# Optimization experiments

Hardware: AMD Instinct MI355X
Metric: run time of the kernel (lower is better)

Reference implementation:

```python
import jax, jax.numpy as jnp
import numpy as np

C = 343.0      # speed of sound (init kwarg c)
F = 16         # number of frequency channels (len(omega))
H = 128        # MLP hidden width
N = 131072     # collocation points


def _mlp(coords, W1, b1, W2, b2, W3, b3):
    # coords: [..., 3] -> [..., 2F] (first F = real part, last F = imag part)
    h = jnp.tanh(coords @ W1 + b1)
    h = jnp.tanh(h @ W2 + b2)
    return h @ W3 + b3


def setup_inputs() -> dict:
    key = jax.random.key(0)
    ks = jax.random.split(key, 4)
    inputs = jax.random.normal(ks[0], (N, 3), dtype=jnp.float32)
    # omega = 2*pi*f for f = 100..1600 Hz (matches init kwarg list)
    omega = 2.0 * jnp.pi * 100.0 * jnp.arange(1, F + 1, dtype=jnp.float32)
    s_in = 1.0 / np.sqrt(3.0)
    s_h = 1.0 / np.sqrt(float(H))
    W1 = jax.random.normal(ks[1], (3, H), dtype=jnp.float32) * s_in
    b1 = jnp.zeros((H,), dtype=jnp.float32)
    W2 = jax.random.normal(ks[2], (H, H), dtype=jnp.float32) * s_h
    b2 = jnp.zeros((H,), dtype=jnp.float32)
    W3 = jax.random.normal(ks[3], (H, 2 * F), dtype=jnp.float32) * s_h
    b3 = jnp.zeros((2 * F,), dtype=jnp.float32)
    return {"inputs": inputs, "omega": omega, "W1": W1, "b1": b1,
            "W2": W2, "b2": b2, "W3": W3, "b3": b3}


def reference(inputs, omega, W1, b1, W2, b2, W3, b3):
    # Pointwise network R^3 -> R^{2F} (real/imag stacked).
    f = lambda c3: _mlp(c3, W1, b1, W2, b2, W3, b3)

    # u: complex pressure per point per frequency, [N, F]
    out = _mlp(inputs, W1, b1, W2, b2, W3, b3)           # [N, 2F]
    u = out[:, :F] + 1j * out[:, F:]

    # Full spatial Hessian per point via forward-over-reverse AD (fused
    # replacement for the torch per-channel autograd.grad loop).
    hess = jax.vmap(jax.jacfwd(jax.jacrev(f)))(inputs)   # [N, 2F, 3, 3]
    lap_ri = jnp.einsum('nfii->nf', hess)                # diagonal trace = Laplacian
    lap = lap_ri[:, :F] + 1j * lap_ri[:, F:]             # [N, F] complex

    # PDE residual skips channel 0, exactly as the torch loop (i+1 indexing).
    k2 = (omega[1:] / C) ** 2                            # [F-1]
    residual = lap[:, 1:] + k2 * u[:, 1:]                # [N, F-1]

    # mean over channels then over batch == global mean of |residual|^2
    return jnp.mean(jnp.abs(residual) ** 2)
```

## Files before the change

### kernel.cpp

```cpp
#include <hip/hip_runtime.h>
#include <math.h>

#ifndef __has_builtin
#define __has_builtin(x) 0
#endif

#define NPTS   131072
#define FCH    16
#define CSND   343.0f
#define PB     32
#define BLOCK  256
#define GRID   1024
#define NBLK   (NPTS / PB)

typedef _Float16 half8 __attribute__((ext_vector_type(8)));
typedef _Float16 half2v __attribute__((ext_vector_type(2)));
typedef float    f32x4 __attribute__((ext_vector_type(4)));

static __device__ __forceinline__ half2v pk2h(float a, float b) {
#if __has_builtin(__builtin_amdgcn_cvt_pkrtz)
  return __builtin_bit_cast(half2v, __builtin_amdgcn_cvt_pkrtz(a, b));
#else
  half2v v; v[0] = (_Float16)a; v[1] = (_Float16)b;
  return v;
#endif
}
static __device__ __forceinline__ unsigned pack2(float a, float b) {
  return __builtin_bit_cast(unsigned, pk2h(a, b));
}
#define U32(h) __builtin_bit_cast(unsigned, (h))

static __device__ __forceinline__ float mytanh(float x) {
#if __has_builtin(__builtin_amdgcn_exp2f)
  float e = __builtin_amdgcn_exp2f(2.885390082f * x);
#else
  float e = __expf(2.0f * x);
#endif
  return fmaf(-2.0f, __builtin_amdgcn_rcpf(e + 1.0f), 1.0f);
}


__global__ __launch_bounds__(BLOCK, 2) void helmholtz_kernel(
    const float* __restrict__ x,
    const float* __restrict__ omega,
    const float* __restrict__ W1,
    const float* __restrict__ b1,
    const float* __restrict__ W2,
    const float* __restrict__ b2,
    const float* __restrict__ W3,
    const float* __restrict__ b3,
    float* __restrict__ out)
{
  __shared__ unsigned s_A[160 * 64];

  {
    int k = (blockIdx.x >> 8) & 3;
    for (int i = 0; i < k; i++) __builtin_amdgcn_s_sleep(63);
  }

  const int tid  = threadIdx.x;
  const int w    = tid >> 6;
  const int l    = tid & 63;
  const int col  = l & 15;
  const int quad = l >> 4;
  const int ph   = w >> 1;
  const int nh   = w & 1;

  const int pA = tid >> 4;
  const int g  = tid & 15;
  float wx[8], wy[8], wz[8], bB[8];
#pragma unroll
  for (int u = 0; u < 8; u++) {
    int unit = 8 * g + u;
    wx[u] = W1[unit]; wy[u] = W1[128 + unit]; wz[u] = W1[256 + unit];
    bB[u] = b1[unit];
  }
  half2v wxp[4], wyp[4], wzp[4], wqm[4];
#pragma unroll
  for (int j = 0; j < 4; j++) {
    wxp[j] = pk2h(wx[2*j], wx[2*j+1]);
    wyp[j] = pk2h(wy[2*j], wy[2*j+1]);
    wzp[j] = pk2h(wz[2*j], wz[2*j+1]);
    float wq0 = fmaf(wx[2*j],   wx[2*j],   fmaf(wy[2*j],   wy[2*j],   wz[2*j]   * wz[2*j]));
    float wq1 = fmaf(wx[2*j+1], wx[2*j+1], fmaf(wy[2*j+1], wy[2*j+1], wz[2*j+1] * wz[2*j+1]));
    wqm[j] = pk2h(-2.0f * wq0, -2.0f * wq1);
  }
  const half2v hone = {(_Float16)1.0f, (_Float16)1.0f};

  half8 w2f[4][4];
#pragma unroll
  for (int t4 = 0; t4 < 4; t4++) {
    const int n = 64 * nh + 16 * t4 + col;
#pragma unroll
    for (int ks = 0; ks < 4; ks++) {
      half8 f;
#pragma unroll
      for (int j8 = 0; j8 < 8; j8++)
        f[j8] = (_Float16)W2[(ks * 32 + (quad << 3) + j8) * 128 + n];
      w2f[t4][ks] = f;
    }
  }
  half8 w3f[4];
#pragma unroll
  for (int ks = 0; ks < 4; ks++) {
    half8 f;
#pragma unroll
    for (int j8 = 0; j8 < 8; j8++) {
      int kap = ks * 32 + (quad << 3) + j8;
      int q   = kap >> 1;
      int j   = 64 * (q >> 5) + 32 * ((q >> 4) & 1) + 16 * (kap & 1) + (q & 15);
      f[j8] = (_Float16)W3[j * 32 + 16 * nh + col];
    }
    w3f[ks] = f;
  }

  float b2r[4];
#pragma unroll
  for (int t4 = 0; t4 < 4; t4++) b2r[t4] = b2[64 * nh + 16 * t4 + col];
  float k2v = 0.0f;
  if (col >= 1) {
    float om = omega[col] * (1.0f / CSND);
    k2v = om * om;
  }
  const float b3v = b3[16 * nh + col];

  float wsum = 0.0f;
  float xr[2][3];

  auto loadX = [&](int blk) {
    const float* xb = x + (size_t)blk * PB * 3;
#pragma unroll
    for (int hp = 0; hp < 2; hp++) {
      int p = pA + 16 * hp;
      xr[hp][0] = xb[3 * p]; xr[hp][1] = xb[3 * p + 1]; xr[hp][2] = xb[3 * p + 2];
    }
  };

  auto phaseA = [&]() {
    const int cbase = (g ^ pA) << 2;
#pragma unroll
    for (int hp = 0; hp < 2; hp++) {
      int p = pA + 16 * hp;
      float x0 = xr[hp][0], x1 = xr[hp][1], x2 = xr[hp][2];
      float t[8];
#pragma unroll
      for (int u = 0; u < 8; u++) {
        float z = fmaf(x0, wx[u], fmaf(x1, wy[u], fmaf(x2, wz[u], bB[u])));
        t[u] = mytanh(z);
      }
      half2v tp[4], sp[4];
#pragma unroll
      for (int j = 0; j < 4; j++) {
        tp[j] = pk2h(t[2*j], t[2*j+1]);
        sp[j] = hone - tp[j] * tp[j];
      }
      uint4 q;
      q = make_uint4(U32(tp[0]), U32(tp[1]), U32(tp[2]), U32(tp[3]));
      *(uint4*)&s_A[(p)       * 64 + cbase] = q;
      q = make_uint4(U32(sp[0]*wxp[0]), U32(sp[1]*wxp[1]),
                     U32(sp[2]*wxp[2]), U32(sp[3]*wxp[3]));
      *(uint4*)&s_A[(32 + p)  * 64 + cbase] = q;
      q = make_uint4(U32(sp[0]*wyp[0]), U32(sp[1]*wyp[1]),
                     U32(sp[2]*wyp[2]), U32(sp[3]*wyp[3]));
      *(uint4*)&s_A[(64 + p)  * 64 + cbase] = q;
      q = make_uint4(U32(sp[0]*wzp[0]), U32(sp[1]*wzp[1]),
                     U32(sp[2]*wzp[2]), U32(sp[3]*wzp[3]));
      *(uint4*)&s_A[(96 + p)  * 64 + cbase] = q;
      half2v cp[4];
#pragma unroll
      for (int j = 0; j < 4; j++) cp[j] = (tp[j] * sp[j]) * wqm[j];
      q = make_uint4(U32(cp[0]), U32(cp[1]), U32(cp[2]), U32(cp[3]));
      *(uint4*)&s_A[(128 + p) * 64 + cbase] = q;
    }
  };

  auto phaseDE = [&]() {
    const int pbase = (16 * ph + col) * 128;
    f32x4 dy = (f32x4){0.0f, 0.0f, 0.0f, 0.0f};
    f32x4 dl = (f32x4){0.0f, 0.0f, 0.0f, 0.0f};
#pragma unroll
    for (int ks = 0; ks < 4; ks++) {
      int pos = ((((ks << 2) + quad) ^ col) << 2);
      half8 afy = *(const half8*)&s_A[pbase + pos];
      half8 afl = *(const half8*)&s_A[pbase + 64 + pos];
      dy = __builtin_amdgcn_mfma_f32_16x16x32_f16(afy, w3f[ks], dy, 0, 0, 0);
      dl = __builtin_amdgcn_mfma_f32_16x16x32_f16(afl, w3f[ks], dl, 0, 0, 0);
    }
    if (col >= 1) {
#pragma unroll
      for (int r = 0; r < 4; r++) {
        float yv  = dy[r] + b3v;
        float res = fmaf(k2v, yv, dl[r]);
        wsum += res * res;
      }
    }
  };

  loadX(blockIdx.x);
  for (int blk = blockIdx.x; blk < NBLK; blk += gridDim.x) {
    phaseA();
    __syncthreads();

    int nblk = blk + (int)gridDim.x;
    if (nblk < NBLK) loadX(nblk);

    f32x4 bsum[4], acch[4], accc[4];
#pragma unroll
    for (int t4 = 0; t4 < 4; t4++)
      bsum[t4] = (f32x4){0.0f, 0.0f, 0.0f, 0.0f};
#pragma unroll
    for (int d = 0; d < 3; d++) {
      f32x4 accd[4];
#pragma unroll
      for (int t4 = 0; t4 < 4; t4++)
        accd[t4] = (f32x4){0.0f, 0.0f, 0.0f, 0.0f};
      const int rb = ((d + 1) * 32 + 16 * ph + col) * 64;
#pragma unroll
      for (int ks = 0; ks < 4; ks++) {
        half8 af = *(const half8*)&s_A[rb + ((((ks << 2) + quad) ^ col) << 2)];
        accd[0] = __builtin_amdgcn_mfma_f32_16x16x32_f16(af, w2f[0][ks], accd[0], 0, 0, 0);
        accd[1] = __builtin_amdgcn_mfma_f32_16x16x32_f16(af, w2f[1][ks], accd[1], 0, 0, 0);
        accd[2] = __builtin_amdgcn_mfma_f32_16x16x32_f16(af, w2f[2][ks], accd[2], 0, 0, 0);
        accd[3] = __builtin_amdgcn_mfma_f32_16x16x32_f16(af, w2f[3][ks], accd[3], 0, 0, 0);
      }
#pragma unroll
      for (int t4 = 0; t4 < 4; t4++)
        bsum[t4] += accd[t4] * accd[t4];
    }
#pragma unroll
    for (int t4 = 0; t4 < 4; t4++) {
      acch[t4] = (f32x4){0.0f, 0.0f, 0.0f, 0.0f};
      accc[t4] = (f32x4){0.0f, 0.0f, 0.0f, 0.0f};
    }
    {
      const int rb0 = (16 * ph + col) * 64;
      const int rb4 = (128 + 16 * ph + col) * 64;
#pragma unroll
      for (int ks = 0; ks < 4; ks++) {
        int pos = ((((ks << 2) + quad) ^ col) << 2);
        half8 afh = *(const half8*)&s_A[rb0 + pos];
        half8 afc = *(const half8*)&s_A[rb4 + pos];
        acch[0] = __builtin_amdgcn_mfma_f32_16x16x32_f16(afh, w2f[0][ks], acch[0], 0, 0, 0);
        acch[1] = __builtin_amdgcn_mfma_f32_16x16x32_f16(afh, w2f[1][ks], acch[1], 0, 0, 0);
        acch[2] = __builtin_amdgcn_mfma_f32_16x16x32_f16(afh, w2f[2][ks], acch[2], 0, 0, 0);
        acch[3] = __builtin_amdgcn_mfma_f32_16x16x32_f16(afh, w2f[3][ks], acch[3], 0, 0, 0);
        accc[0] = __builtin_amdgcn_mfma_f32_16x16x32_f16(afc, w2f[0][ks], accc[0], 0, 0, 0);
        accc[1] = __builtin_amdgcn_mfma_f32_16x16x32_f16(afc, w2f[1][ks], accc[1], 0, 0, 0);
        accc[2] = __builtin_amdgcn_mfma_f32_16x16x32_f16(afc, w2f[2][ks], accc[2], 0, 0, 0);
        accc[3] = __builtin_amdgcn_mfma_f32_16x16x32_f16(afc, w2f[3][ks], accc[3], 0, 0, 0);
      }
    }
    __syncthreads();

#pragma unroll
    for (int r = 0; r < 4; r++) {
      int p = 16 * ph + (quad << 2) + r;
      float t2[4], gg[4];
#pragma unroll
      for (int t4 = 0; t4 < 4; t4++) {
        float z2 = acch[t4][r] + b2r[t4];
        float t  = mytanh(z2);
        float s2 = 1.0f - t * t;
        t2[t4] = t;
        gg[t4] = s2 * (accc[t4][r] - 2.0f * t * bsum[t4][r]);
      }
      int pb = p * 128;
#pragma unroll
      for (int pr = 0; pr < 2; pr++) {
        int q   = 32 * nh + 16 * pr + col;
        int pos = (((q >> 2) ^ (p & 15)) << 2) + (q & 3);
        s_A[pb + pos]      = pack2(t2[2 * pr], t2[2 * pr + 1]);
        s_A[pb + 64 + pos] = pack2(gg[2 * pr], gg[2 * pr + 1]);
      }
    }
    __syncthreads();

    phaseDE();
    __syncthreads();
  }

#pragma unroll
  for (int off = 32; off > 0; off >>= 1)
    wsum += __shfl_down(wsum, off, 64);
  if (l == 0)
    atomicAdd(out, wsum * (1.0f / ((float)NPTS * (float)(FCH - 1))));
}

extern "C" void kernel_launch(void* const* d_in, const int* in_sizes, int n_in,
                              void* d_out, int out_size, void* d_ws, size_t ws_size,
                              hipStream_t stream) {
  const float* x     = (const float*)d_in[0];
  const float* omega = (const float*)d_in[1];
  const float* W1    = (const float*)d_in[2];
  const float* b1    = (const float*)d_in[3];
  const float* W2    = (const float*)d_in[4];
  const float* b2    = (const float*)d_in[5];
  const float* W3    = (const float*)d_in[6];
  const float* b3    = (const float*)d_in[7];
  float* out = (float*)d_out;

  (void)hipMemsetAsync(out, 0, sizeof(float), stream);
  helmholtz_kernel<<<GRID, BLOCK, 0, stream>>>(x, omega, W1, b1, W2, b2, W3, b3, out);
}
```

Baseline: 135.8 us.

## Double-buffer LDS stages and software-pipeline layers with one barrier per tile

Halves the points per tile to 16 and splits the hidden-layer N dimension across all four waves instead of points×halves. Shared memory is double-buffered for both the layer-1 activations and the layer-2 outputs. Phase A for the next tile and the output-layer MFMA for the previous tile are interleaved with the current tile's layer-2 MFMAs, which cuts per-tile barriers from three to one. The trade-offs are more tiles with smaller MFMA work each, only two of four waves doing the final-layer work, a rebalanced W3 fragment mapping, and a changed startup stagger.

```diff
diff --git a/kernel.cpp b/kernel.cpp
--- a/kernel.cpp
+++ b/kernel.cpp
@@ -8,10 +8,13 @@
 #define NPTS   131072
 #define FCH    16
 #define CSND   343.0f
-#define PB     32
+#define PB     16
 #define BLOCK  256
-#define GRID   1024
+#define GRID   512
 #define NBLK   (NPTS / PB)
+
+#define AOFF(k)  ((k) * 5120)
+#define HOFF(k)  (10240 + (k) * 2048)
 
 typedef _Float16 half8 __attribute__((ext_vector_type(8)));
 typedef _Float16 half2v __attribute__((ext_vector_type(2)));
@@ -51,11 +54,11 @@
     const float* __restrict__ b3,
     float* __restrict__ out)
 {
-  __shared__ unsigned s_A[160 * 64];
-
-  {
-    int k = (blockIdx.x >> 8) & 3;
-    for (int i = 0; i < k; i++) __builtin_amdgcn_s_sleep(63);
+  __shared__ unsigned s_mem[14336];
+
+  if ((blockIdx.x >> 8) & 1) {
+#pragma unroll
+    for (int i = 0; i < 3; i++) __builtin_amdgcn_s_sleep(48);
   }
 
   const int tid  = threadIdx.x;
@@ -63,7 +66,6 @@
   const int l    = tid & 63;
   const int col  = l & 15;
   const int quad = l >> 4;
-  const int ph   = w >> 1;
   const int nh   = w & 1;
 
   const int pA = tid >> 4;
@@ -87,17 +89,17 @@
   }
   const half2v hone = {(_Float16)1.0f, (_Float16)1.0f};
 
-  half8 w2f[4][4];
-#pragma unroll
-  for (int t4 = 0; t4 < 4; t4++) {
-    const int n = 64 * nh + 16 * t4 + col;
+  half8 w2f[2][4];
+#pragma unroll
+  for (int nt = 0; nt < 2; nt++) {
+    const int n = 32 * w + 16 * nt + col;
 #pragma unroll
     for (int ks = 0; ks < 4; ks++) {
       half8 f;
 #pragma unroll
       for (int j8 = 0; j8 < 8; j8++)
         f[j8] = (_Float16)W2[(ks * 32 + (quad << 3) + j8) * 128 + n];
-      w2f[t4][ks] = f;
+      w2f[nt][ks] = f;
     }
   }
   half8 w3f[4];
@@ -106,17 +108,15 @@
     half8 f;
 #pragma unroll
     for (int j8 = 0; j8 < 8; j8++) {
-      int kap = ks * 32 + (quad << 3) + j8;
-      int q   = kap >> 1;
-      int j   = 64 * (q >> 5) + 32 * ((q >> 4) & 1) + 16 * (kap & 1) + (q & 15);
+      int j = 32 * ks + 16 * (j8 & 1) + 4 * quad + (j8 >> 1);
       f[j8] = (_Float16)W3[j * 32 + 16 * nh + col];
     }
     w3f[ks] = f;
   }
 
-  float b2r[4];
-#pragma unroll
-  for (int t4 = 0; t4 < 4; t4++) b2r[t4] = b2[64 * nh + 16 * t4 + col];
+  float b2r[2];
+#pragma unroll
+  for (int nt = 0; nt < 2; nt++) b2r[nt] = b2[32 * w + 16 * nt + col];
   float k2v = 0.0f;
   if (col >= 1) {
     float om = omega[col] * (1.0f / CSND);
@@ -125,159 +125,161 @@
   const float b3v = b3[16 * nh + col];
 
   float wsum = 0.0f;
-  float xr[2][3];
-
-  auto loadX = [&](int blk) {
+  float xrC[3], xrN[3];
+
+  auto loadX = [&](int blk, float* xr) {
     const float* xb = x + (size_t)blk * PB * 3;
-#pragma unroll
-    for (int hp = 0; hp < 2; hp++) {
-      int p = pA + 16 * hp;
-      xr[hp][0] = xb[3 * p]; xr[hp][1] = xb[3 * p + 1]; xr[hp][2] = xb[3 * p + 2];
-    }
+    xr[0] = xb[3 * pA]; xr[1] = xb[3 * pA + 1]; xr[2] = xb[3 * pA + 2];
   };
 
-  auto phaseA = [&]() {
-    const int cbase = (g ^ pA) << 2;
-#pragma unroll
-    for (int hp = 0; hp < 2; hp++) {
-      int p = pA + 16 * hp;
-      float x0 = xr[hp][0], x1 = xr[hp][1], x2 = xr[hp][2];
-      float t[8];
-#pragma unroll
-      for (int u = 0; u < 8; u++) {
-        float z = fmaf(x0, wx[u], fmaf(x1, wy[u], fmaf(x2, wz[u], bB[u])));
-        t[u] = mytanh(z);
-      }
-      half2v tp[4], sp[4];
-#pragma unroll
-      for (int j = 0; j < 4; j++) {
-        tp[j] = pk2h(t[2*j], t[2*j+1]);
-        sp[j] = hone - tp[j] * tp[j];
-      }
-      uint4 q;
-      q = make_uint4(U32(tp[0]), U32(tp[1]), U32(tp[2]), U32(tp[3]));
-      *(uint4*)&s_A[(p)       * 64 + cbase] = q;
-      q = make_uint4(U32(sp[0]*wxp[0]), U32(sp[1]*wxp[1]),
-                     U32(sp[2]*wxp[2]), U32(sp[3]*wxp[3]));
-      *(uint4*)&s_A[(32 + p)  * 64 + cbase] = q;
-      q = make_uint4(U32(sp[0]*wyp[0]), U32(sp[1]*wyp[1]),
-                     U32(sp[2]*wyp[2]), U32(sp[3]*wyp[3]));
-      *(uint4*)&s_A[(64 + p)  * 64 + cbase] = q;
-      q = make_uint4(U32(sp[0]*wzp[0]), U32(sp[1]*wzp[1]),
-                     U32(sp[2]*wzp[2]), U32(sp[3]*wzp[3]));
-      *(uint4*)&s_A[(96 + p)  * 64 + cbase] = q;
-      half2v cp[4];
-#pragma unroll
-      for (int j = 0; j < 4; j++) cp[j] = (tp[j] * sp[j]) * wqm[j];
-      q = make_uint4(U32(cp[0]), U32(cp[1]), U32(cp[2]), U32(cp[3]));
-      *(uint4*)&s_A[(128 + p) * 64 + cbase] = q;
-    }
+  auto phaseA = [&](int aOff, const float* xr) {
+    const int cbase = ((g ^ pA) << 2) + aOff;
+    float x0 = xr[0], x1 = xr[1], x2 = xr[2];
+    float t[8];
+#pragma unroll
+    for (int u = 0; u < 8; u++) {
+      float z = fmaf(x0, wx[u], fmaf(x1, wy[u], fmaf(x2, wz[u], bB[u])));
+      t[u] = mytanh(z);
+    }
+    half2v tp[4], sp[4];
+#pragma unroll
+    for (int j = 0; j < 4; j++) {
+      tp[j] = pk2h(t[2*j], t[2*j+1]);
+      sp[j] = hone - tp[j] * tp[j];
+    }
+    uint4 q;
+    q = make_uint4(U32(tp[0]), U32(tp[1]), U32(tp[2]), U32(tp[3]));
+    *(uint4*)&s_mem[(pA)      * 64 + cbase] = q;
+    q = make_uint4(U32(sp[0]*wxp[0]), U32(sp[1]*wxp[1]),
+                   U32(sp[2]*wxp[2]), U32(sp[3]*wxp[3]));
+    *(uint4*)&s_mem[(16 + pA) * 64 + cbase] = q;
+    q = make_uint4(U32(sp[0]*wyp[0]), U32(sp[1]*wyp[1]),
+                   U32(sp[2]*wyp[2]), U32(sp[3]*wyp[3]));
+    *(uint4*)&s_mem[(32 + pA) * 64 + cbase] = q;
+    q = make_uint4(U32(sp[0]*wzp[0]), U32(sp[1]*wzp[1]),
+                   U32(sp[2]*wzp[2]), U32(sp[3]*wzp[3]));
+    *(uint4*)&s_mem[(48 + pA) * 64 + cbase] = q;
+    half2v cp[4];
+#pragma unroll
+    for (int j = 0; j < 4; j++) cp[j] = (tp[j] * sp[j]) * wqm[j];
+    q = make_uint4(U32(cp[0]), U32(cp[1]), U32(cp[2]), U32(cp[3]));
+    *(uint4*)&s_mem[(64 + pA) * 64 + cbase] = q;
   };
 
-  auto phaseDE = [&]() {
-    const int pbase = (16 * ph + col) * 128;
-    f32x4 dy = (f32x4){0.0f, 0.0f, 0.0f, 0.0f};
-    f32x4 dl = (f32x4){0.0f, 0.0f, 0.0f, 0.0f};
-#pragma unroll
-    for (int ks = 0; ks < 4; ks++) {
-      int pos = ((((ks << 2) + quad) ^ col) << 2);
-      half8 afy = *(const half8*)&s_A[pbase + pos];
-      half8 afl = *(const half8*)&s_A[pbase + 64 + pos];
-      dy = __builtin_amdgcn_mfma_f32_16x16x32_f16(afy, w3f[ks], dy, 0, 0, 0);
-      dl = __builtin_amdgcn_mfma_f32_16x16x32_f16(afl, w3f[ks], dl, 0, 0, 0);
-    }
-    if (col >= 1) {
-#pragma unroll
-      for (int r = 0; r < 4; r++) {
-        float yv  = dy[r] + b3v;
-        float res = fmaf(k2v, yv, dl[r]);
-        wsum += res * res;
+  auto phaseD = [&](int hOff) {
+    if (w < 2) {
+      const int pbase = hOff + col * 128;
+      f32x4 dy = (f32x4){0.0f, 0.0f, 0.0f, 0.0f};
+      f32x4 dl = (f32x4){0.0f, 0.0f, 0.0f, 0.0f};
+#pragma unroll
+      for (int ks = 0; ks < 4; ks++) {
+        int pos = ((((ks << 2) + quad) ^ col) << 2);
+        half8 afy = *(const half8*)&s_mem[pbase + pos];
+        half8 afl = *(const half8*)&s_mem[pbase + 64 + pos];
+        dy = __builtin_amdgcn_mfma_f32_16x16x32_f16(afy, w3f[ks], dy, 0, 0, 0);
+        dl = __builtin_amdgcn_mfma_f32_16x16x32_f16(afl, w3f[ks], dl, 0, 0, 0);
+      }
+      if (col >= 1) {
+#pragma unroll
+        for (int r = 0; r < 4; r++) {
+          float yv  = dy[r] + b3v;
+          float res = fmaf(k2v, yv, dl[r]);
+          wsum += res * res;
+        }
       }
     }
   };
 
-  loadX(blockIdx.x);
-  for (int blk = blockIdx.x; blk < NBLK; blk += gridDim.x) {
-    phaseA();
-    __syncthreads();
-
-    int nblk = blk + (int)gridDim.x;
-    if (nblk < NBLK) loadX(nblk);
-
-    f32x4 bsum[4], acch[4], accc[4];
-#pragma unroll
-    for (int t4 = 0; t4 < 4; t4++)
-      bsum[t4] = (f32x4){0.0f, 0.0f, 0.0f, 0.0f};
+  loadX(blockIdx.x, xrC);
+  phaseA(AOFF(0), xrC);
+  {
+    int nb = blockIdx.x + GRID;
+    if (nb < NBLK) loadX(nb, xrN);
+  }
+  __syncthreads();
+
+  bool hasPrev = false;
+  int cur = 0;
+  for (int blk = blockIdx.x; blk < NBLK; blk += GRID) {
+    int nblk = blk + GRID;
+    if (nblk < NBLK) {
+      xrC[0] = xrN[0]; xrC[1] = xrN[1]; xrC[2] = xrN[2];
+      int n2 = nblk + GRID;
+      if (n2 < NBLK) loadX(n2, xrN);
+      phaseA(AOFF(cur ^ 1), xrC);
+    }
+    if (hasPrev) phaseD(HOFF(cur ^ 1));
+
+    const int aOff = AOFF(cur);
+    f32x4 bsum[2], acch[2], accc[2];
+#pragma unroll
+    for (int nt = 0; nt < 2; nt++)
+      bsum[nt] = (f32x4){0.0f, 0.0f, 0.0f, 0.0f};
 #pragma unroll
     for (int d = 0; d < 3; d++) {
-      f32x4 accd[4];
-#pragma unroll
-      for (int t4 = 0; t4 < 4; t4++)
-        accd[t4] = (f32x4){0.0f, 0.0f, 0.0f, 0.0f};
-      const int rb = ((d + 1) * 32 + 16 * ph + col) * 64;
+      f32x4 accd[2];
+#pragma unroll
+      for (int nt = 0; nt < 2; nt++)
+        accd[nt] = (f32x4){0.0f, 0.0f, 0.0f, 0.0f};
+      const int rb = aOff + ((d + 1) * 16 + col) * 64;
 #pragma unroll
       for (int ks = 0; ks < 4; ks++) {
-        half8 af = *(const half8*)&s_A[rb + ((((ks << 2) + quad) ^ col) << 2)];
+        half8 af = *(const half8*)&s_mem[rb + ((((ks << 2) + quad) ^ col) << 2)];
         accd[0] = __builtin_amdgcn_mfma_f32_16x16x32_f16(af, w2f[0][ks], accd[0], 0, 0, 0);
         accd[1] = __builtin_amdgcn_mfma_f32_16x16x32_f16(af, w2f[1][ks], accd[1], 0, 0, 0);
-        accd[2] = __builtin_amdgcn_mfma_f32_16x16x32_f16(af, w2f[2][ks], accd[2], 0, 0, 0);
-        accd[3] = __builtin_amdgcn_mfma_f32_16x16x32_f16(af, w2f[3][ks], accd[3], 0, 0, 0);
-      }
-#pragma unroll
-      for (int t4 = 0; t4 < 4; t4++)
-        bsum[t4] += accd[t4] * accd[t4];
-    }
-#pragma unroll
-    for (int t4 = 0; t4 < 4; t4++) {
-      acch[t4] = (f32x4){0.0f, 0.0f, 0.0f, 0.0f};
-      accc[t4] = (f32x4){0.0f, 0.0f, 0.0f, 0.0f};
+      }
+#pragma unroll
+      for (int nt = 0; nt < 2; nt++)
+        bsum[nt] += accd[nt] * accd[nt];
+    }
+#pragma unroll
+    for (int nt = 0; nt < 2; nt++) {
+      acch[nt] = (f32x4){0.0f, 0.0f, 0.0f, 0.0f};
+      accc[nt] = (f32x4){0.0f, 0.0f, 0.0f, 0.0f};
     }
     {
-      const int rb0 = (16 * ph + col) * 64;
-      const int rb4 = (128 + 16 * ph + col) * 64;
+      const int rb0 = aOff + (col) * 64;
+      const int rb4 = aOff + (64 + col) * 64;
 #pragma unroll
       for (int ks = 0; ks < 4; ks++) {
         int pos = ((((ks << 2) + quad) ^ col) << 2);
-        half8 afh = *(const half8*)&s_A[rb0 + pos];
-        half8 afc = *(const half8*)&s_A[rb4 + pos];
+        half8 afh = *(const half8*)&s_mem[rb0 + pos];
+        half8 afc = *(const half8*)&s_mem[rb4 + pos];
         acch[0] = __builtin_amdgcn_mfma_f32_16x16x32_f16(afh, w2f[0][ks], acch[0], 0, 0, 0);
         acch[1] = __builtin_amdgcn_mfma_f32_16x16x32_f16(afh, w2f[1][ks], acch[1], 0, 0, 0);
-        acch[2] = __builtin_amdgcn_mfma_f32_16x16x32_f16(afh, w2f[2][ks], acch[2], 0, 0, 0);
-        acch[3] = __builtin_amdgcn_mfma_f32_16x16x32_f16(afh, w2f[3][ks], acch[3], 0, 0, 0);
         accc[0] = __builtin_amdgcn_mfma_f32_16x16x32_f16(afc, w2f[0][ks], accc[0], 0, 0, 0);
         accc[1] = __builtin_amdgcn_mfma_f32_16x16x32_f16(afc, w2f[1][ks], accc[1], 0, 0, 0);
-        accc[2] = __builtin_amdgcn_mfma_f32_16x16x32_f16(afc, w2f[2][ks], accc[2], 0, 0, 0);
-        accc[3] = __builtin_amdgcn_mfma_f32_16x16x32_f16(afc, w2f[3][ks], accc[3], 0, 0, 0);
-      }
-    }
+      }
+    }
+
+    {
+      const int hOff = HOFF(cur);
+      const int q    = 16 * w + col;
+      const int qc   = q >> 2, qr = q & 3;
+#pragma unroll
+      for (int r = 0; r < 4; r++) {
+        int p = (quad << 2) + r;
+        float t2[2], gg[2];
+#pragma unroll
+        for (int nt = 0; nt < 2; nt++) {
+          float z2 = acch[nt][r] + b2r[nt];
+          float t  = mytanh(z2);
+          float s2 = 1.0f - t * t;
+          t2[nt] = t;
+          gg[nt] = s2 * (accc[nt][r] - 2.0f * t * bsum[nt][r]);
+        }
+        int pos = ((qc ^ p) << 2) + qr;
+        int pb  = hOff + p * 128;
+        s_mem[pb + pos]      = pack2(t2[0], t2[1]);
+        s_mem[pb + 64 + pos] = pack2(gg[0], gg[1]);
+      }
+    }
+
+    hasPrev = true;
     __syncthreads();
-
-#pragma unroll
-    for (int r = 0; r < 4; r++) {
-      int p = 16 * ph + (quad << 2) + r;
-      float t2[4], gg[4];
-#pragma unroll
-      for (int t4 = 0; t4 < 4; t4++) {
-        float z2 = acch[t4][r] + b2r[t4];
-        float t  = mytanh(z2);
-        float s2 = 1.0f - t * t;
-        t2[t4] = t;
-        gg[t4] = s2 * (accc[t4][r] - 2.0f * t * bsum[t4][r]);
-      }
-      int pb = p * 128;
-#pragma unroll
-      for (int pr = 0; pr < 2; pr++) {
-        int q   = 32 * nh + 16 * pr + col;
-        int pos = (((q >> 2) ^ (p & 15)) << 2) + (q & 3);
-        s_A[pb + pos]      = pack2(t2[2 * pr], t2[2 * pr + 1]);
-        s_A[pb + 64 + pos] = pack2(gg[2 * pr], gg[2 * pr + 1]);
-      }
-    }
-    __syncthreads();
-
-    phaseDE();
-    __syncthreads();
-  }
+    cur ^= 1;
+  }
+  phaseD(HOFF(cur ^ 1));
 
 #pragma unroll
   for (int off = 32; off > 0; off >>= 1)
```

After: 118.2 us. -12.9%, faster.
